# Optimization experiments

Hardware: AMD Instinct MI355X
Metric: run time of the kernel (lower is better)

The kernel has to match this reference:

```python
import jax, jax.numpy as jnp
import numpy as np

D_MODEL = 1024
NUM_HEADS = 16
D_K = D_MODEL // NUM_HEADS
ROPE_THETA = 10000.0
BATCH = 4
SEQ = 2048


def _trunc_normal(key, shape):
    # approx of torch.nn.init.trunc_normal_ (std=1, truncated to [-2, 2])
    return jnp.clip(jax.random.truncated_normal(key, -2.0, 2.0, shape, jnp.float32), -2.0, 2.0)


def setup_inputs() -> dict:
    key = jax.random.key(0)
    kx, kq, kk, kv, ko = jax.random.split(key, 5)
    x = jax.random.normal(kx, (BATCH, SEQ, D_MODEL), jnp.float32)
    token_positions = jnp.broadcast_to(jnp.arange(SEQ, dtype=jnp.int32), (BATCH, SEQ))
    return {
        "x": x,
        "token_positions": token_positions,
        "q_proj": _trunc_normal(kq, (D_MODEL, D_MODEL)),
        "k_proj": _trunc_normal(kk, (D_MODEL, D_MODEL)),
        "v_proj": _trunc_normal(kv, (D_MODEL, D_MODEL)),
        "o_proj": _trunc_normal(ko, (D_MODEL, D_MODEL)),
    }


def _rope(t, positions):
    # t: [b, h, s, k], positions: [b, s]
    half = D_K // 2
    inv_freq = 1.0 / (ROPE_THETA ** (jnp.arange(half, dtype=jnp.float32) * 2.0 / D_K))
    ang = positions.astype(jnp.float32)[:, None, :, None] * inv_freq  # [b,1,s,half]
    cos, sin = jnp.cos(ang), jnp.sin(ang)
    t1 = t[..., 0::2]
    t2 = t[..., 1::2]
    r1 = t1 * cos - t2 * sin
    r2 = t1 * sin + t2 * cos
    return jnp.stack([r1, r2], axis=-1).reshape(t.shape)


def reference(x, token_positions, q_proj, k_proj, v_proj, o_proj):
    b, s, d = x.shape
    Wq = q_proj.reshape(NUM_HEADS, D_K, d)
    Wk = k_proj.reshape(NUM_HEADS, D_K, d)
    Wv = v_proj.reshape(NUM_HEADS, D_K, d)
    Wo = o_proj.reshape(d, NUM_HEADS, D_K).transpose(1, 0, 2)  # h d k
    Q = jnp.einsum('bsd,hkd->bhsk', x, Wq)
    K = jnp.einsum('bsd,hkd->bhsk', x, Wk)
    V = jnp.einsum('bsd,hkd->bhsk', x, Wv)
    Q = _rope(Q, token_positions)
    K = _rope(K, token_positions)
    scale = 1.0 / jnp.sqrt(jnp.asarray(D_K, jnp.float32))
    scores = jnp.einsum('bhqk,bhsk->bhqs', Q, K) * scale  # [b,h,s,s]
    causal = jnp.tril(jnp.ones((s, s), dtype=bool))
    scores = jnp.where(causal, scores, -jnp.inf)
    attn = jax.nn.softmax(scores, axis=-1)
    O = jnp.einsum('bhqs,bhsk->bhqk', attn, V)
    return jnp.einsum('bhsk,hdk->bsd', O, Wo)
```

## Files before the change

kernel.cpp:

```cpp
#include <hip/hip_runtime.h>
#include <cmath>


typedef __bf16 bf16_t;
typedef __bf16 bf16x2 __attribute__((ext_vector_type(2)));
typedef __bf16 bf16x4 __attribute__((ext_vector_type(4)));
typedef __bf16 bf16x8 __attribute__((ext_vector_type(8)));
typedef float f32x2 __attribute__((ext_vector_type(2)));
typedef float f32x4 __attribute__((ext_vector_type(4)));
typedef unsigned int u32;
typedef const __attribute__((address_space(1))) u32* gaddr_t;
typedef __attribute__((address_space(3))) u32* saddr_t;

struct RopeTab { float inv[32]; };

__device__ __forceinline__ void split4(const float* __restrict__ in,
                                       bf16_t* __restrict__ hi,
                                       bf16_t* __restrict__ lo, bool LO,
                                       int blk, int tid)
{
  const int i = blk * 256 + tid;
  const f32x4 u = *(const f32x4*)(in + (size_t)i * 4);
  bf16x4 h, l;
  #pragma unroll
  for (int j = 0; j < 4; ++j) {
    const bf16_t hb = (bf16_t)u[j];
    h[j] = hb;
    if (LO) l[j] = (bf16_t)(u[j] - (float)hb);
  }
  *(bf16x4*)(hi + (size_t)i * 4) = h;
  if (LO) *(bf16x4*)(lo + (size_t)i * 4) = l;
}

__global__ __launch_bounds__(256) void prep_k(
    const float* __restrict__ x,  const float* __restrict__ qw,
    const float* __restrict__ kw, const float* __restrict__ vw,
    const float* __restrict__ ow, RopeTab tab,
    bf16_t* __restrict__ Xh,  bf16_t* __restrict__ Xl,
    bf16_t* __restrict__ QWh, bf16_t* __restrict__ QWl,
    bf16_t* __restrict__ KWh, bf16_t* __restrict__ KWl,
    bf16_t* __restrict__ VWh, bf16_t* __restrict__ OWh,
    float* __restrict__ ropeT)
{
  const int bid = blockIdx.x, tid = threadIdx.x;
  if (bid < 8192)       split4(x,  Xh,  Xl,  true,  bid,         tid);
  else if (bid < 9216)  split4(qw, QWh, QWl, true,  bid - 8192,  tid);
  else if (bid < 10240) split4(kw, KWh, KWl, true,  bid - 9216,  tid);
  else if (bid < 11264) split4(vw, VWh, nullptr, false, bid - 10240, tid);
  else if (bid < 12288) split4(ow, OWh, nullptr, false, bid - 11264, tid);
  else {
    const int i = (bid - 12288) * 256 + tid;
    const int p = i >> 5, d2 = i & 31;
    float sn, cs;
    sincosf((float)p * tab.inv[d2], &sn, &cs);
    ropeT[(size_t)i * 2]     = cs;
    ropeT[(size_t)i * 2 + 1] = sn;
  }
}

__global__ __launch_bounds__(512, 1) void gemm_qk256(
    const bf16_t* __restrict__ Xh, const bf16_t* __restrict__ Xl,
    const bf16_t* __restrict__ QWh, const bf16_t* __restrict__ QWl,
    const bf16_t* __restrict__ KWh, const bf16_t* __restrict__ KWl,
    const int* __restrict__ tokpos, const float* __restrict__ ropeT,
    bf16_t* __restrict__ Oq_h, bf16_t* __restrict__ Oq_l,
    bf16_t* __restrict__ Ok_h, bf16_t* __restrict__ Ok_l)
{
  __shared__ __align__(16) bf16_t sA[2][256 * 64];
  __shared__ __align__(16) bf16_t sB[2][256 * 64];

  const int tid = threadIdx.x;
  const int lane = tid & 63, wv = tid >> 6;
  const int wr = wv >> 2, wc = wv & 3;
  const int la = lane & 15, lb = lane >> 4;

  const int lin  = (int)blockIdx.y * 32 + (int)blockIdx.x;
  const int lin2 = (lin & 7) * 16 + (lin >> 3);
  const int bx = lin2 & 31, by = lin2 >> 5;
  const int row0 = bx * 256, col0 = by * 256;
  const int z = blockIdx.z;

  const bf16_t* Wh = z ? KWh : QWh;
  const bf16_t* Wl = z ? KWl : QWl;

  const int sr8  = tid >> 3;
  const int scsw = (tid & 7) ^ (sr8 & 7);

  f32x4 acc[8][4] = {};

  auto STAGE = [&](int t, int buf) {
    const int seg = t >> 4;
    const int k0 = (t & 15) << 6;
    const bf16_t* Ap = (seg == 2) ? Xl : Xh;
    const bf16_t* Wp = (seg == 1) ? Wl : Wh;
    #pragma unroll
    for (int j = 0; j < 4; ++j) {
      const int r = j * 64 + sr8;
      __builtin_amdgcn_global_load_lds(
          (gaddr_t)(Ap + (size_t)(row0 + r) * 1024 + k0 + scsw * 8),
          (saddr_t)(&sA[buf][0] + j * 4096 + tid * 8), 16, 0, 0);
    }
    #pragma unroll
    for (int j = 0; j < 4; ++j) {
      const int r = j * 64 + sr8;
      __builtin_amdgcn_global_load_lds(
          (gaddr_t)(Wp + (size_t)(col0 + r) * 1024 + k0 + scsw * 8),
          (saddr_t)(&sB[buf][0] + j * 4096 + tid * 8), 16, 0, 0);
    }
  };

  const int NT = 48;
  STAGE(0, 0);
  for (int t = 0; t < NT; ++t) {
    if (t + 1 < NT) {
      STAGE(t + 1, (t + 1) & 1);
      asm volatile("s_waitcnt vmcnt(8)" ::: "memory");
    } else {
      asm volatile("s_waitcnt vmcnt(0)" ::: "memory");
    }
    __builtin_amdgcn_s_barrier();

    const bf16_t* cA = &sA[t & 1][0];
    const bf16_t* cB = &sB[t & 1][0];
    #pragma unroll
    for (int ks = 0; ks < 2; ++ks) {
      bf16x8 bfr[4];
      #pragma unroll
      for (int nf = 0; nf < 4; ++nf) {
        const int r = wc * 64 + nf * 16 + la;
        bfr[nf] = *(const bf16x8*)&cB[r * 64 + (((ks * 4 + lb) ^ (la & 7)) * 8)];
      }
      __builtin_amdgcn_s_setprio(1);
      #pragma unroll
      for (int mf = 0; mf < 8; ++mf) {
        const int r = wr * 128 + mf * 16 + la;
        const bf16x8 a = *(const bf16x8*)&cA[r * 64 + (((ks * 4 + lb) ^ (la & 7)) * 8)];
        #pragma unroll
        for (int nf = 0; nf < 4; ++nf)
          acc[mf][nf] = __builtin_amdgcn_mfma_f32_16x16x32_bf16(a, bfr[nf], acc[mf][nf], 0, 0, 0);
      }
      __builtin_amdgcn_s_setprio(0);
    }
    __builtin_amdgcn_s_barrier();
  }

  bf16_t* Oh = z ? Ok_h : Oq_h;
  bf16_t* Ol = z ? Ok_l : Oq_l;
  #pragma unroll
  for (int n = 0; n < 4; ++n) {
    const int gn = col0 + wc * 64 + n * 16 + la;
    const int d = gn & 63, h = gn >> 6;
    const bool odd = d & 1;
    #pragma unroll
    for (int m = 0; m < 8; ++m) {
      const int gm0 = row0 + wr * 128 + m * 16 + lb * 4;
      #pragma unroll
      for (int j = 0; j < 4; ++j) {
        const int gm = gm0 + j;
        const float t = acc[m][n][j];
        const float other = __shfl_xor(t, 1, 64);
        const int pos = tokpos[gm];
        const f32x2 cs2 = *(const f32x2*)&ropeT[((size_t)pos << 6) + ((d >> 1) << 1)];
        const float r = odd ? (other * cs2[1] + t * cs2[0])
                            : (t * cs2[0] - other * cs2[1]);
        const bf16_t hb = (bf16_t)r;
        const int b = gm >> 11, s = gm & 2047;
        const size_t oi = (((size_t)b * 16 + h) * 2048 + s) * 64 + d;
        Oh[oi] = hb;
        Ol[oi] = (bf16_t)(r - (float)hb);
      }
    }
  }
}

__global__ __launch_bounds__(256, 4) void gemm_qkv(
    const bf16_t* __restrict__ Xh, const bf16_t* __restrict__ Xl,
    const bf16_t* __restrict__ QWh, const bf16_t* __restrict__ QWl,
    const bf16_t* __restrict__ KWh, const bf16_t* __restrict__ KWl,
    const bf16_t* __restrict__ VWh,
    const int* __restrict__ tokpos, const float* __restrict__ ropeT,
    bf16_t* __restrict__ Oq_h, bf16_t* __restrict__ Oq_l,
    bf16_t* __restrict__ Ok_h, bf16_t* __restrict__ Ok_l,
    bf16_t* __restrict__ Vt, int zbase)
{
  __shared__ __align__(16) bf16_t sA[128 * 64];
  __shared__ __align__(16) bf16_t sB[128 * 64];

  const int tid = threadIdx.x;
  const int lane = tid & 63, wv = tid >> 6;
  const int wr = wv >> 1, wc = wv & 1;
  const int la = lane & 15, lb = lane >> 4;
  const int row0 = blockIdx.x * 128, col0 = blockIdx.y * 128;
  const int z = blockIdx.z + zbase;

  const int srow = wv * 32 + (lane >> 3);
  const int schk = lane & 7;

  f32x4 acc[4][4] = {};

  const int NT = (z == 2) ? 16 : 48;

  for (int t = 0; t < NT; ++t) {
    const int seg = t >> 4;
    const int k0 = (t & 15) << 6;
    const bf16_t* Ap = (z < 2 && seg == 2) ? Xl : Xh;
    const bf16_t* Wp = (z == 2) ? VWh
                     : (z == 1) ? ((seg == 1) ? KWl : KWh)
                                : ((seg == 1) ? QWl : QWh);
    __syncthreads();
    #pragma unroll
    for (int i = 0; i < 4; ++i) {
      const int r = srow + i * 8;
      const int cs_ = (schk ^ (r & 7)) * 8;
      __builtin_amdgcn_global_load_lds(
          (gaddr_t)(Ap + (size_t)(row0 + r) * 1024 + k0 + cs_),
          (saddr_t)(sA + wv * 2048 + i * 512), 16, 0, 0);
      __builtin_amdgcn_global_load_lds(
          (gaddr_t)(Wp + (size_t)(col0 + r) * 1024 + k0 + cs_),
          (saddr_t)(sB + wv * 2048 + i * 512), 16, 0, 0);
    }
    __syncthreads();

    #pragma unroll
    for (int ks = 0; ks < 2; ++ks) {
      bf16x8 af[4];
      #pragma unroll
      for (int m = 0; m < 4; ++m) {
        const int r = wr * 64 + m * 16 + la;
        af[m] = *(const bf16x8*)&sA[r * 64 + (((ks * 4 + lb) ^ (la & 7)) * 8)];
      }
      #pragma unroll
      for (int n = 0; n < 4; ++n) {
        const int r = wc * 64 + n * 16 + la;
        const bf16x8 bfr = *(const bf16x8*)&sB[r * 64 + (((ks * 4 + lb) ^ (la & 7)) * 8)];
        #pragma unroll
        for (int m = 0; m < 4; ++m)
          acc[m][n] = __builtin_amdgcn_mfma_f32_16x16x32_bf16(af[m], bfr, acc[m][n], 0, 0, 0);
      }
    }
  }

  #pragma unroll
  for (int n = 0; n < 4; ++n) {
    const int gn = col0 + wc * 64 + n * 16 + la;
    #pragma unroll
    for (int m = 0; m < 4; ++m) {
      const int gm0 = row0 + wr * 64 + m * 16 + lb * 4;
      if (z == 2) {
        const int b = gm0 >> 11, s0 = gm0 & 2047;
        const int h = gn >> 6, d = gn & 63;
        bf16x4 v;
        #pragma unroll
        for (int j = 0; j < 4; ++j) v[j] = (bf16_t)acc[m][n][j];
        *(bf16x4*)&Vt[(((size_t)b * 16 + h) * 64 + d) * 2048 + s0] = v;
      } else {
        const int d = gn & 63, h = gn >> 6;
        const bool odd = d & 1;
        bf16_t* Oh = z ? Ok_h : Oq_h;
        bf16_t* Ol = z ? Ok_l : Oq_l;
        #pragma unroll
        for (int j = 0; j < 4; ++j) {
          const int gm = gm0 + j;
          const float t = acc[m][n][j];
          const float other = __shfl_xor(t, 1, 64);
          const int pos = tokpos[gm];
          const f32x2 cs2 = *(const f32x2*)&ropeT[((size_t)pos << 6) + ((d >> 1) << 1)];
          const float r = odd ? (other * cs2[1] + t * cs2[0])
                              : (t * cs2[0] - other * cs2[1]);
          const bf16_t hb = (bf16_t)r;
          const int b = gm >> 11, s = gm & 2047;
          const size_t oi = (((size_t)b * 16 + h) * 2048 + s) * 64 + d;
          Oh[oi] = hb;
          Ol[oi] = (bf16_t)(r - (float)hb);
        }
      }
    }
  }
}

__global__ __launch_bounds__(256, 4) void gemm_o(
    const bf16_t* __restrict__ Ag, const bf16_t* __restrict__ Wg,
    float* __restrict__ Of)
{
  __shared__ __align__(16) bf16_t sA[128 * 64];
  __shared__ __align__(16) bf16_t sB[128 * 64];

  const int tid = threadIdx.x;
  const int lane = tid & 63, wv = tid >> 6;
  const int wr = wv >> 1, wc = wv & 1;
  const int la = lane & 15, lb = lane >> 4;
  const int row0 = blockIdx.x * 128, col0 = blockIdx.y * 128;

  const int srow = wv * 32 + (lane >> 3);
  const int schk = lane & 7;

  f32x4 acc[4][4] = {};

  for (int t = 0; t < 16; ++t) {
    const int k0 = t << 6;
    __syncthreads();
    #pragma unroll
    for (int i = 0; i < 4; ++i) {
      const int r = srow + i * 8;
      const int cs_ = (schk ^ (r & 7)) * 8;
      __builtin_amdgcn_global_load_lds(
          (gaddr_t)(Ag + (size_t)(row0 + r) * 1024 + k0 + cs_),
          (saddr_t)(sA + wv * 2048 + i * 512), 16, 0, 0);
      __builtin_amdgcn_global_load_lds(
          (gaddr_t)(Wg + (size_t)(col0 + r) * 1024 + k0 + cs_),
          (saddr_t)(sB + wv * 2048 + i * 512), 16, 0, 0);
    }
    __syncthreads();
    #pragma unroll
    for (int ks = 0; ks < 2; ++ks) {
      bf16x8 af[4];
      #pragma unroll
      for (int m = 0; m < 4; ++m) {
        const int r = wr * 64 + m * 16 + la;
        af[m] = *(const bf16x8*)&sA[r * 64 + (((ks * 4 + lb) ^ (la & 7)) * 8)];
      }
      #pragma unroll
      for (int n = 0; n < 4; ++n) {
        const int r = wc * 64 + n * 16 + la;
        const bf16x8 bfr = *(const bf16x8*)&sB[r * 64 + (((ks * 4 + lb) ^ (la & 7)) * 8)];
        #pragma unroll
        for (int m = 0; m < 4; ++m)
          acc[m][n] = __builtin_amdgcn_mfma_f32_16x16x32_bf16(af[m], bfr, acc[m][n], 0, 0, 0);
      }
    }
  }

  #pragma unroll
  for (int n = 0; n < 4; ++n) {
    const int gn = col0 + wc * 64 + n * 16 + la;
    #pragma unroll
    for (int m = 0; m < 4; ++m) {
      const int gm0 = row0 + wr * 64 + m * 16 + lb * 4;
      #pragma unroll
      for (int j = 0; j < 4; ++j)
        Of[(size_t)(gm0 + j) * 1024 + gn] = acc[m][n][j];
    }
  }
}

__device__ __forceinline__ int SW(int e) { return e ^ (((e >> 6) & 7) << 3); }

__global__ __launch_bounds__(512, 4) void attn_kernel(
    const bf16_t* __restrict__ Qhi, const bf16_t* __restrict__ Qlo,
    const bf16_t* __restrict__ Khi, const bf16_t* __restrict__ Klo,
    const bf16_t* __restrict__ Vt, bf16_t* __restrict__ O)
{
  __shared__ __align__(16) bf16_t sKV[2][3 * 4096];
  __shared__ __align__(16) bf16_t sP[8 * 1024];

  const int linear = (int)blockIdx.x;
  const int xcd = linear & 7;
  const int pos = linear >> 3;
  const int bh  = xcd * 8 + (pos >> 3);
  const int p   = pos & 7;
  const int b = bh >> 4, h = bh & 15;

  const size_t base = (size_t)bh * 2048 * 64;
  const bf16_t* Qh_ = Qhi + base;
  const bf16_t* Ql_ = Qlo + base;
  const bf16_t* Kh_ = Khi + base;
  const bf16_t* Kl_ = Klo + base;
  const bf16_t* Vt_ = Vt + base;

  const int tid = threadIdx.x, wv = tid >> 6, lane = tid & 63;
  const int la = lane & 15, lb = lane >> 4;

  const int sr   = wv * 8 + (lane >> 3);
  const int scsw = (lane & 7) ^ (sr & 7);
  const int ssrc = sr * 64 + scsw * 8;
  const int se0  = wv * 512;
  const int psw  = (la & 7) << 3;

  auto STAGE = [&](int kvb, int buf) {
    const int kv0 = kvb * 64;
    bf16_t* dst = &sKV[buf][0];
    __builtin_amdgcn_global_load_lds((gaddr_t)(Kh_ + (size_t)kv0 * 64 + ssrc),
                                     (saddr_t)(dst + se0), 16, 0, 0);
    __builtin_amdgcn_global_load_lds((gaddr_t)(Kl_ + (size_t)kv0 * 64 + ssrc),
                                     (saddr_t)(dst + 4096 + se0), 16, 0, 0);
    __builtin_amdgcn_global_load_lds((gaddr_t)(Vt_ + (size_t)sr * 2048 + kv0 + scsw * 8),
                                     (saddr_t)(dst + 8192 + se0), 16, 0, 0);
  };

  for (int half = 0; half < 2; ++half) {
    const int qb = half ? p : 15 - p;
    const int q = qb * 128 + wv * 16 + la;
    bf16x8 qh[2], ql[2];
    #pragma unroll
    for (int kf = 0; kf < 2; ++kf) {
      qh[kf] = *(const bf16x8*)&Qh_[(size_t)q * 64 + kf * 32 + lb * 8];
      ql[kf] = *(const bf16x8*)&Ql_[(size_t)q * 64 + kf * 32 + lb * 8];
    }

    f32x4 oacc[4] = {};
    float m = -1e30f, l = 0.f;
    const int nt = 2 * qb + 2;

    STAGE(0, 0);
    __syncthreads();

    for (int kvb = 0; kvb < nt; ++kvb) {
      const int kv0 = kvb * 64;
      if (kvb + 1 < nt) STAGE(kvb + 1, (kvb + 1) & 1);

      const bf16_t* sKh = &sKV[kvb & 1][0];
      const bf16_t* sKl = sKh + 4096;
      const bf16_t* sVt = sKh + 8192;

      f32x4 sacc[4] = {};
      __builtin_amdgcn_s_setprio(1);
      #pragma unroll
      for (int nf = 0; nf < 4; ++nf) {
        #pragma unroll
        for (int kf = 0; kf < 2; ++kf) {
          const int rr = SW((nf * 16 + la) * 64 + kf * 32 + lb * 8);
          const bf16x8 kh = *(const bf16x8*)&sKh[rr];
          const bf16x8 kl = *(const bf16x8*)&sKl[rr];
          sacc[nf] = __builtin_amdgcn_mfma_f32_16x16x32_bf16(kh, qh[kf], sacc[nf], 0, 0, 0);
          sacc[nf] = __builtin_amdgcn_mfma_f32_16x16x32_bf16(kl, qh[kf], sacc[nf], 0, 0, 0);
          sacc[nf] = __builtin_amdgcn_mfma_f32_16x16x32_bf16(kh, ql[kf], sacc[nf], 0, 0, 0);
        }
      }
      __builtin_amdgcn_s_setprio(0);

      if (kvb >= 2 * qb) {
        #pragma unroll
        for (int nf = 0; nf < 4; ++nf)
          #pragma unroll
          for (int j = 0; j < 4; ++j) {
            const int kvi = kv0 + nf * 16 + lb * 4 + j;
            sacc[nf][j] = (kvi <= q) ? sacc[nf][j] * 0.125f : -1e30f;
          }
      } else {
        #pragma unroll
        for (int nf = 0; nf < 4; ++nf)
          #pragma unroll
          for (int j = 0; j < 4; ++j) sacc[nf][j] *= 0.125f;
      }

      float red = sacc[0][0];
      #pragma unroll
      for (int nf = 0; nf < 4; ++nf)
        #pragma unroll
        for (int j = 0; j < 4; ++j) red = fmaxf(red, sacc[nf][j]);
      red = fmaxf(red, __shfl_xor(red, 16, 64));
      red = fmaxf(red, __shfl_xor(red, 32, 64));

      const float mn = fmaxf(m, red);
      if (!__all(mn - m <= 8.0f)) {
        const float sf = __expf(m - mn);
        m = mn;
        l *= sf;
        #pragma unroll
        for (int nf = 0; nf < 4; ++nf)
          #pragma unroll
          for (int j = 0; j < 4; ++j) oacc[nf][j] *= sf;
      }

      float rs = 0.f;
      #pragma unroll
      for (int nf = 0; nf < 4; ++nf)
        #pragma unroll
        for (int j = 0; j < 4; ++j) {
          const float pj = __expf(sacc[nf][j] - m);
          sacc[nf][j] = pj;
          rs += pj;
        }
      rs += __shfl_xor(rs, 16, 64);
      rs += __shfl_xor(rs, 32, 64);
      l += rs;

      #pragma unroll
      for (int nf = 0; nf < 4; ++nf) {
        bf16x4 pv;
        #pragma unroll
        for (int j = 0; j < 4; ++j) pv[j] = (bf16_t)sacc[nf][j];
        *(bf16x4*)&sP[wv * 1024 + la * 64 + ((nf * 16 + lb * 4) ^ psw)] = pv;
      }

      __builtin_amdgcn_s_setprio(1);
      #pragma unroll
      for (int ks = 0; ks < 2; ++ks) {
        const bf16x8 pa = *(const bf16x8*)&sP[wv * 1024 + la * 64 + ((ks * 32 + lb * 8) ^ psw)];
        #pragma unroll
        for (int nf = 0; nf < 4; ++nf) {
          const bf16x8 vb2 = *(const bf16x8*)&sVt[SW((nf * 16 + la) * 64 + ks * 32 + lb * 8)];
          oacc[nf] = __builtin_amdgcn_mfma_f32_16x16x32_bf16(vb2, pa, oacc[nf], 0, 0, 0);
        }
      }
      __builtin_amdgcn_s_setprio(0);

      __syncthreads();
    }

    const float inv_l = 1.0f / l;
    #pragma unroll
    for (int nf = 0; nf < 4; ++nf) {
      bf16x4 ov;
      #pragma unroll
      for (int j = 0; j < 4; ++j) ov[j] = (bf16_t)(oacc[nf][j] * inv_l);
      const int d0 = nf * 16 + lb * 4;
      *(bf16x4*)&O[(((size_t)b * 2048 + q) * 16 + h) * 64 + d0] = ov;
    }
  }
}

extern "C" void kernel_launch(void* const* d_in, const int* in_sizes, int n_in,
                              void* d_out, int out_size, void* d_ws, size_t ws_size,
                              hipStream_t stream)
{
  const float* x      = (const float*)d_in[0];
  const int*   tokpos = (const int*)d_in[1];
  const float* qw     = (const float*)d_in[2];
  const float* kw     = (const float*)d_in[3];
  const float* vw     = (const float*)d_in[4];
  const float* ow     = (const float*)d_in[5];
  float* out = (float*)d_out;

  const size_t E  = (size_t)4 * 16 * 2048 * 64;
  const size_t W1 = (size_t)1024 * 1024;
  bf16_t* base = (bf16_t*)d_ws;
  bf16_t* Qhi = base;
  bf16_t* Qlo = base + E;
  bf16_t* Khi = base + 2 * E;
  bf16_t* Klo = base + 3 * E;
  bf16_t* Vt  = base + 4 * E;
  bf16_t* Xh  = base + 5 * E;
  bf16_t* Xl  = base + 6 * E;
  bf16_t* QWh = base + 7 * E;
  bf16_t* QWl = QWh + W1;
  bf16_t* KWh = QWh + 2 * W1;
  bf16_t* KWl = QWh + 3 * W1;
  bf16_t* VWh = QWh + 4 * W1;
  bf16_t* OWh = QWh + 5 * W1;
  float*  ropeT = (float*)(QWh + 6 * W1);
  bf16_t* O = Xh;

  RopeTab tab;
  for (int i = 0; i < 32; ++i)
    tab.inv[i] = (float)pow(10000.0, -(double)i / 32.0);

  prep_k<<<12544, 256, 0, stream>>>(x, qw, kw, vw, ow, tab,
                                    Xh, Xl, QWh, QWl, KWh, KWl, VWh, OWh, ropeT);

  gemm_qk256<<<dim3(32, 4, 2), 512, 0, stream>>>(
      Xh, Xl, QWh, QWl, KWh, KWl, tokpos, ropeT, Qhi, Qlo, Khi, Klo);
  gemm_qkv<<<dim3(64, 8, 1), 256, 0, stream>>>(
      Xh, Xl, QWh, QWl, KWh, KWl, VWh, tokpos, ropeT,
      Qhi, Qlo, Khi, Klo, Vt, 2);
  attn_kernel<<<512, 512, 0, stream>>>(Qhi, Qlo, Khi, Klo, Vt, O);
  gemm_o<<<dim3(64, 8), 256, 0, stream>>>(O, OWh, out);
}
```

Baseline: 282.0 us.

## Interleave next-tile global-to-LDS loads with MFMA phases in QK projection GEMM

Splits each K-tile's LDS staging into four quarter-loads and the MFMA work into four phases (two k-steps times two M halves). Each phase issues one quarter of the next tile's loads, so global traffic is spread across the compute instead of issued in one burst. This aims to overlap memory with MFMA more evenly and to lower register pressure by holding only half the A fragments at once. In exchange it adds more barriers per tile, and the finer-grained waitcnt scheduling could serialize waves.

New measurement: 289.0 us. +2.5%, slower.

```diff
diff --git a/kernel.cpp b/kernel.cpp
--- a/kernel.cpp
+++ b/kernel.cpp
@@ -88,60 +88,77 @@
 
   f32x4 acc[8][4] = {};
 
-  auto STAGE = [&](int t, int buf) {
+  auto STAGE_H = [&](int t, int buf, int h) {
     const int seg = t >> 4;
     const int k0 = (t & 15) << 6;
-    const bf16_t* Ap = (seg == 2) ? Xl : Xh;
-    const bf16_t* Wp = (seg == 1) ? Wl : Wh;
-    #pragma unroll
-    for (int j = 0; j < 4; ++j) {
-      const int r = j * 64 + sr8;
+    const bf16_t* src = (h < 2) ? ((seg == 2) ? Xl : Xh)
+                                : ((seg == 1) ? Wl : Wh);
+    bf16_t* dstb = (h < 2) ? &sA[buf][0] : &sB[buf][0];
+    const int base_ = (h < 2) ? row0 : col0;
+    const int half = h & 1;
+    #pragma unroll
+    for (int j = 0; j < 2; ++j) {
+      const int jr = half * 2 + j;
+      const int r = jr * 64 + sr8;
       __builtin_amdgcn_global_load_lds(
-          (gaddr_t)(Ap + (size_t)(row0 + r) * 1024 + k0 + scsw * 8),
-          (saddr_t)(&sA[buf][0] + j * 4096 + tid * 8), 16, 0, 0);
-    }
-    #pragma unroll
-    for (int j = 0; j < 4; ++j) {
-      const int r = j * 64 + sr8;
-      __builtin_amdgcn_global_load_lds(
-          (gaddr_t)(Wp + (size_t)(col0 + r) * 1024 + k0 + scsw * 8),
-          (saddr_t)(&sB[buf][0] + j * 4096 + tid * 8), 16, 0, 0);
+          (gaddr_t)(src + (size_t)(base_ + r) * 1024 + k0 + scsw * 8),
+          (saddr_t)(dstb + jr * 4096 + tid * 8), 16, 0, 0);
     }
   };
 
   const int NT = 48;
-  STAGE(0, 0);
+  #pragma unroll
+  for (int h = 0; h < 4; ++h) STAGE_H(0, 0, h);
+
   for (int t = 0; t < NT; ++t) {
-    if (t + 1 < NT) {
-      STAGE(t + 1, (t + 1) & 1);
-      asm volatile("s_waitcnt vmcnt(8)" ::: "memory");
-    } else {
-      asm volatile("s_waitcnt vmcnt(0)" ::: "memory");
-    }
-    __builtin_amdgcn_s_barrier();
-
-    const bf16_t* cA = &sA[t & 1][0];
-    const bf16_t* cB = &sB[t & 1][0];
-    #pragma unroll
-    for (int ks = 0; ks < 2; ++ks) {
-      bf16x8 bfr[4];
-      #pragma unroll
-      for (int nf = 0; nf < 4; ++nf) {
-        const int r = wc * 64 + nf * 16 + la;
-        bfr[nf] = *(const bf16x8*)&cB[r * 64 + (((ks * 4 + lb) ^ (la & 7)) * 8)];
-      }
+    const int buf = t & 1, nbuf = buf ^ 1;
+    const bf16_t* cA = &sA[buf][0];
+    const bf16_t* cB = &sB[buf][0];
+    bf16x8 bfr[4];
+
+    #pragma unroll
+    for (int p = 0; p < 4; ++p) {
+      const int ks = p >> 1, mh = p & 1;
+      bf16x8 afr[4];
+      const int kcol = ((ks * 4 + lb) ^ (la & 7)) * 8;
+
+      if (p == 0) {
+        if (t + 1 < NT) {
+          STAGE_H(t + 1, nbuf, 0);
+          asm volatile("s_waitcnt vmcnt(2)" ::: "memory");
+        } else {
+          asm volatile("s_waitcnt vmcnt(0)" ::: "memory");
+        }
+        __builtin_amdgcn_s_barrier();
+        #pragma unroll
+        for (int nf = 0; nf < 4; ++nf)
+          bfr[nf] = *(const bf16x8*)&cB[(wc * 64 + nf * 16 + la) * 64 + kcol];
+        #pragma unroll
+        for (int i = 0; i < 4; ++i)
+          afr[i] = *(const bf16x8*)&cA[(wr * 128 + i * 16 + la) * 64 + kcol];
+      } else {
+        if (mh == 0) {
+          #pragma unroll
+          for (int nf = 0; nf < 4; ++nf)
+            bfr[nf] = *(const bf16x8*)&cB[(wc * 64 + nf * 16 + la) * 64 + kcol];
+        }
+        #pragma unroll
+        for (int i = 0; i < 4; ++i)
+          afr[i] = *(const bf16x8*)&cA[(wr * 128 + (mh * 4 + i) * 16 + la) * 64 + kcol];
+        if (t + 1 < NT) STAGE_H(t + 1, nbuf, p);
+        __builtin_amdgcn_s_barrier();
+      }
+
       __builtin_amdgcn_s_setprio(1);
       #pragma unroll
-      for (int mf = 0; mf < 8; ++mf) {
-        const int r = wr * 128 + mf * 16 + la;
-        const bf16x8 a = *(const bf16x8*)&cA[r * 64 + (((ks * 4 + lb) ^ (la & 7)) * 8)];
+      for (int i = 0; i < 4; ++i)
         #pragma unroll
         for (int nf = 0; nf < 4; ++nf)
-          acc[mf][nf] = __builtin_amdgcn_mfma_f32_16x16x32_bf16(a, bfr[nf], acc[mf][nf], 0, 0, 0);
-      }
+          acc[mh * 4 + i][nf] =
+              __builtin_amdgcn_mfma_f32_16x16x32_bf16(afr[i], bfr[nf], acc[mh * 4 + i][nf], 0, 0, 0);
       __builtin_amdgcn_s_setprio(0);
-    }
-    __builtin_amdgcn_s_barrier();
+      __builtin_amdgcn_s_barrier();
+    }
   }
 
   bf16_t* Oh = z ? Ok_h : Oq_h;
```
